# Kernel tuning notes

Measured on AMD Instinct MI355X. Metric: run time of the kernel, lower is better.

## Reference

```python
import jax, jax.numpy as jnp
import numpy as np

D_MODEL = 1024
N_HEADS = 16
HEAD_DIM = D_MODEL // N_HEADS  # 64
GRID = 8  # 8x8 Ising grid over head_dim pixels
N_DIFF_STEPS = 2
STEPS_PER_SAMPLE = 8  # cfg sampling.steps_per_sample
BETA_START = 0.8
BETA_END = 1.2


def setup_inputs() -> dict:
    key = jax.random.key(0)
    k1, k2, k3 = jax.random.split(key, 3)
    B, N = 4, 4096
    q = jax.random.normal(k1, (B, N, D_MODEL), dtype=jnp.float32)
    k = jax.random.normal(k2, (B, N, D_MODEL), dtype=jnp.float32)
    v = jax.random.normal(k3, (B, N, D_MODEL), dtype=jnp.float32)
    return {"q": q, "k": k, "v": v}


def _nbr_field(s):
    # s: (..., G, G) spins in {-1, +1}; 4-neighbor sum with open (non-torus) boundary
    zr = jnp.zeros_like(s[..., :1, :])
    zc = jnp.zeros_like(s[..., :, :1])
    up = jnp.concatenate([s[..., 1:, :], zr], axis=-2)
    down = jnp.concatenate([zr, s[..., :-1, :]], axis=-2)
    left = jnp.concatenate([s[..., :, 1:], zc], axis=-1)
    right = jnp.concatenate([zc, s[..., :, :-1]], axis=-1)
    return up + down + left + right


def _fta_forward(v):
    B, N, D = v.shape
    H, HD = N_HEADS, HEAD_DIM
    # binarize values -> Ising spins per head: (B, H, N, G, G)
    vh = v.reshape(B, N, H, HD).transpose(0, 2, 1, 3)
    spins = jnp.where(vh > 0, 1.0, -1.0).astype(jnp.float32).reshape(B, H, N, GRID, GRID)

    # log-spaced beta schedule (diffusion_schedule kind='log'), each diffusion
    # step runs STEPS_PER_SAMPLE Gibbs sweeps
    betas = jnp.exp(jnp.linspace(jnp.log(BETA_START), jnp.log(BETA_END), N_DIFF_STEPS))
    betas = jnp.repeat(betas, STEPS_PER_SAMPLE)  # (T,)
    T = N_DIFF_STEPS * STEPS_PER_SAMPLE

    ii, jj = jnp.meshgrid(jnp.arange(GRID), jnp.arange(GRID), indexing="ij")
    parity = ((ii + jj) % 2).astype(jnp.float32)  # checkerboard mask (G, G)

    keys = jax.random.split(jax.random.key(1234), T)

    def gibbs_step(s, xs):
        beta, kk = xs
        k0, k1 = jax.random.split(kk)

        def half_sweep(s, mask, kh):
            h = _nbr_field(s)
            p = jax.nn.sigmoid(2.0 * beta * h)  # P(spin=+1 | neighbors)
            u = jax.random.uniform(kh, s.shape, dtype=s.dtype)
            new = jnp.where(u < p, 1.0, -1.0)
            return jnp.where(mask > 0.5, new, s)

        s = half_sweep(s, parity, k0)
        s = half_sweep(s, 1.0 - parity, k1)
        return s, None

    spins, _ = jax.lax.scan(gibbs_step, spins, (betas, keys))

    # back to (B, N, D); spins already in {-1, +1} == bool*2-1
    out = spins.reshape(B, H, N, HD).transpose(0, 2, 1, 3).reshape(B, N, D)
    return out


def reference(q, k, v):
    # q and k are accepted for interface fidelity but, as in the source
    # module's head_fta, only v participates in the computation.
    return _fta_forward(v)
```

## Files before the change

kernel.cpp:

```cpp
#include <hip/hip_runtime.h>
#include <stdint.h>
#include <string.h>
#include <math.h>


struct FtaParams {
  uint32_t hk[32][2];
  uint32_t K9[2][9];
};

static inline void tf2x32_host(uint32_t k0, uint32_t k1, uint32_t c0, uint32_t c1,
                               uint32_t& o0, uint32_t& o1) {
  uint32_t ks2 = k0 ^ k1 ^ 0x1BD11BDAu;
  uint32_t x0 = c0 + k0, x1 = c1 + k1;
#define TFR(r) { x0 += x1; x1 = (x1 << (r)) | (x1 >> (32 - (r))); x1 ^= x0; }
  TFR(13) TFR(15) TFR(26) TFR(6)
  x0 += k1;  x1 += ks2 + 1u;
  TFR(17) TFR(29) TFR(16) TFR(24)
  x0 += ks2; x1 += k0 + 2u;
  TFR(13) TFR(15) TFR(26) TFR(6)
  x0 += k0;  x1 += k1 + 3u;
  TFR(17) TFR(29) TFR(16) TFR(24)
  x0 += k1;  x1 += ks2 + 4u;
  TFR(13) TFR(15) TFR(26) TFR(6)
  x0 += ks2; x1 += k0 + 5u;
#undef TFR
  o0 = x0; o1 = x1;
}

__device__ __forceinline__ static void tf_bits4(
    uint32_t K0, uint32_t K1, uint32_t ks2,
    uint32_t i1, uint32_t i2, uint32_t i3, uint32_t i4, uint32_t i5,
    uint32_t m0, uint32_t m1, uint32_t m2, uint32_t m3,
    uint32_t& o0, uint32_t& o1, uint32_t& o2, uint32_t& o3) {
#define ROTL(x, r) __builtin_amdgcn_alignbit((x), (x), 32u - (r))
#define QR4(r)                                                             \
  a0 += a1; b0 += b1; c0 += c1; d0 += d1;                                  \
  a1 = ROTL(a1, r) ^ a0; b1 = ROTL(b1, r) ^ b0;                            \
  c1 = ROTL(c1, r) ^ c0; d1 = ROTL(d1, r) ^ d0;
#define INJ4(sx, si)                                                       \
  a0 += sx; b0 += sx; c0 += sx; d0 += sx;                                  \
  a1 += si; b1 += si; c1 += si; d1 += si;
  uint32_t a1 = m0, b1 = m1, c1 = m2, d1 = m3;
  uint32_t a0 = K0 + a1, b0 = K0 + b1, c0 = K0 + c1, d0 = K0 + d1;
  a1 = ROTL(a1, 13) ^ a0; b1 = ROTL(b1, 13) ^ b0;
  c1 = ROTL(c1, 13) ^ c0; d1 = ROTL(d1, 13) ^ d0;
  QR4(15) QR4(26) QR4(6)
  INJ4(K1, i1)
  QR4(17) QR4(29) QR4(16) QR4(24)
  INJ4(ks2, i2)
  QR4(13) QR4(15) QR4(26) QR4(6)
  INJ4(K0, i3)
  QR4(17) QR4(29) QR4(16) QR4(24)
  INJ4(K1, i4)
  QR4(13) QR4(15) QR4(26) QR4(6)
  a0 += ks2; b0 += ks2; c0 += ks2; d0 += ks2;
  a1 += i5;  b1 += i5;  c1 += i5;  d1 += i5;
  o0 = a0 ^ a1; o1 = b0 ^ b1; o2 = c0 ^ c1; o3 = d0 ^ d1;
#undef QR4
#undef INJ4
#undef ROTL
}

__global__ __launch_bounds__(256, 8) void fta_kernel(const float* __restrict__ v,
                                                     float* __restrict__ out,
                                                     FtaParams P) {
  uint32_t tid = blockIdx.x * 256u + threadIdx.x;
  const int half = (int)(tid & 1u);
  uint32_t g = tid >> 1;
  uint32_t b = g >> 16;
  uint32_t h = (g >> 12) & 15u;
  uint32_t n = g & 4095u;

  size_t voff = ((size_t)(b * 4096u + n)) * 1024u + (size_t)h * 64u
              + (size_t)(half * 32);

  uint32_t nat = 0u;
#pragma unroll
  for (int k = 0; k < 32; k += 4) {
    float4 a = *reinterpret_cast<const float4*>(v + voff + k);
    nat |= ((uint32_t)(a.x > 0.0f)) << (k + 0);
    nat |= ((uint32_t)(a.y > 0.0f)) << (k + 1);
    nat |= ((uint32_t)(a.z > 0.0f)) << (k + 2);
    nat |= ((uint32_t)(a.w > 0.0f)) << (k + 3);
  }
  uint32_t bd = half ? __brev(nat) : nat;

  const uint32_t mgrid = g * 64u;
  const uint32_t mpc = mgrid + (half ? 63u : 0u);
  const int sgn = half ? -1 : 1;

  uint32_t K[9];
#pragma unroll
  for (int q = 0; q < 9; ++q) K[q] = P.K9[0][q];

  const uint32_t PM[2] = { 0x55AA55AAu, 0xAA55AA55u };

  for (int t = 0; t < 16; ++t) {
    if (t == 8) {
#pragma unroll
      for (int q = 0; q < 9; ++q) K[q] = P.K9[1][q];
    }
#pragma unroll
    for (int hf = 0; hf < 2; ++hf) {
      const uint32_t K0 = P.hk[2 * t + hf][0];
      const uint32_t K1 = P.hk[2 * t + hf][1];
      const uint32_t ks2 = K0 ^ K1 ^ 0x1BD11BDAu;
      const uint32_t i1 = ks2 + 1u, i2 = K0 + 2u, i3 = K1 + 3u,
                     i4 = ks2 + 4u, i5 = K0 + 5u;
      const uint32_t cKp = mpc + K1;

      uint32_t myrow3 = bd >> 24;
      uint32_t xrow = (uint32_t)__shfl_xor((int)myrow3, 1, 64);
      uint32_t xb = __brev(xrow) >> 24;

      uint32_t U  = (bd >> 8) | (xb << 24);
      uint32_t D  = bd << 8;
      uint32_t Lp = (bd >> 1) & 0x7f7f7f7fu;
      uint32_t Rp = (bd << 1) & 0xfefefefeu;
      uint32_t t0 = U ^ D,  ca = U & D;
      uint32_t t1 = Lp ^ Rp, cb = Lp & Rp;
      uint32_t c0 = t0 ^ t1, cc = t0 & t1;
      uint32_t cx = ca ^ cb;
      uint32_t c1 = cx ^ cc;
      uint32_t c2 = (ca & cb) | (cc & cx);

      uint32_t acc = 0u;
#pragma unroll
      for (int lr = 0; lr < 4; ++lr) {
        const int j0 = (lr + 1 + hf) & 1;
        const int L0 = lr * 8 + j0;
        uint32_t bits[4];
        tf_bits4(K0, K1, ks2, i1, i2, i3, i4, i5,
                 (uint32_t)((int)cKp + sgn * (L0 + 0)),
                 (uint32_t)((int)cKp + sgn * (L0 + 2)),
                 (uint32_t)((int)cKp + sgn * (L0 + 4)),
                 (uint32_t)((int)cKp + sgn * (L0 + 6)),
                 bits[0], bits[1], bits[2], bits[3]);
#pragma unroll
        for (int jj = 0; jj < 4; ++jj) {
          const int lc = j0 + 2 * jj;
          const int L = lr * 8 + lc;
          uint32_t b0v = (c0 >> L) & 1u;
          uint32_t b1v = (c1 >> L) & 1u;
          const int e = (int)(lr == 0) + (int)(lc == 0) + (int)(lc == 7);
          uint32_t thr;
          if (e == 0) {
            uint32_t b2v = (c2 >> L) & 1u;
            uint32_t tA = b0v ? K[2] : K[0];
            uint32_t tB = b0v ? K[6] : K[4];
            uint32_t tC = b1v ? tB : tA;
            thr = b2v ? K[8] : tC;
          } else if (e == 1) {
            uint32_t tA = b0v ? K[3] : K[1];
            uint32_t tB = b0v ? K[7] : K[5];
            thr = b1v ? tB : tA;
          } else {
            uint32_t tA = b0v ? K[4] : K[2];
            thr = b1v ? K[6] : tA;
          }
          uint32_t nb = (bits[jj] < thr) ? 1u : 0u;
          acc |= nb << L;
        }
      }
      bd = (bd & ~PM[hf]) | acc;
    }
  }

  uint32_t nato = half ? __brev(bd) : bd;
#pragma unroll
  for (int k = 0; k < 32; k += 4) {
    float4 o;
    o.x = ((nato >> (k + 0)) & 1u) ? 1.0f : -1.0f;
    o.y = ((nato >> (k + 1)) & 1u) ? 1.0f : -1.0f;
    o.z = ((nato >> (k + 2)) & 1u) ? 1.0f : -1.0f;
    o.w = ((nato >> (k + 3)) & 1u) ? 1.0f : -1.0f;
    *reinterpret_cast<float4*>(out + voff + k) = o;
  }
}

static float xla_expf(float xin) {
  const float exp_hi = 88.3762626647950f;
  const float exp_lo = -88.3762626647949f;
  const float LOG2EF = 1.44269504088896341f;
  const float C1 = 0.693359375f;
  const float C2 = -2.12194440e-4f;
  const float Pc0 = 1.9875691500E-4f;
  const float Pc1 = 1.3981999507E-3f;
  const float Pc2 = 8.3334519073E-3f;
  const float Pc3 = 4.1665795894E-2f;
  const float Pc4 = 1.6666665459E-1f;
  const float Pc5 = 5.0000001201E-1f;
#define MA(a, b, c) ((a) * (b) + (c))
  float x = xin;
  if (x > exp_hi) x = exp_hi;
  if (x < exp_lo) x = exp_lo;
  float fx = floorf(MA(x, LOG2EF, 0.5f));
  float tmp = C1 * fx;
  float z = C2 * fx;
  x = x - tmp;
  x = x - z;
  z = x * x;
  float y = MA(x, Pc0, Pc1);
  y = MA(y, x, Pc2);
  y = MA(y, x, Pc3);
  y = MA(y, x, Pc4);
  y = MA(y, x, Pc5);
  y = MA(y, z, x);
  y = y + 1.0f;
  int nn = (int)fx;
  uint32_t eb = (uint32_t)(nn + 127) << 23;
  float p2n;
  memcpy(&p2n, &eb, 4);
  float r = y * p2n;
  return r > xin ? r : xin;
#undef MA
}

extern "C" void kernel_launch(void* const* d_in, const int* in_sizes, int n_in,
                              void* d_out, int out_size, void* d_ws, size_t ws_size,
                              hipStream_t stream) {
  (void)in_sizes; (void)n_in; (void)d_ws; (void)ws_size; (void)out_size;
  const float* v = (const float*)d_in[2];
  float* out = (float*)d_out;

  FtaParams P;

  const uint32_t rk0 = 0u, rk1 = 1234u;
  uint32_t kt[16][2];
  for (uint32_t t = 0; t < 16; ++t) tf2x32_host(rk0, rk1, 0u, t, kt[t][0], kt[t][1]);
  for (int t = 0; t < 16; ++t) {
    uint32_t a0, a1, b0, b1;
    tf2x32_host(kt[t][0], kt[t][1], 0u, 0u, a0, a1);
    tf2x32_host(kt[t][0], kt[t][1], 0u, 1u, b0, b1);
    P.hk[2 * t + 0][0] = a0; P.hk[2 * t + 0][1] = a1;
    P.hk[2 * t + 1][0] = b0; P.hk[2 * t + 1][1] = b1;
  }

  float bet[2];
  bet[0] = (float)exp((double)(float)log((double)0.8f));
  bet[1] = (float)exp((double)(float)log((double)1.2f));

  for (int s = 0; s < 2; ++s) {
    float x2b = 2.0f * bet[s];
    for (int hh = -4; hh <= 4; ++hh) {
      float xh = x2b * (float)hh;
      float e = xla_expf(-xh);
      float p = 1.0f / (1.0f + e);
      double pd = (double)p * 8388608.0;
      uint64_t kc = (uint64_t)ceil(pd);
      uint64_t k9 = kc << 9;
      P.K9[s][hh + 4] = (k9 > 0xFFFFFFFFull) ? 0xFFFFFFFFu : (uint32_t)k9;
    }
  }

  fta_kernel<<<dim3(2048), dim3(256), 0, stream>>>(v, out, P);
}
```

Measured before the change: 529.8 us.

## Replace register-select threshold lookup with shared-memory table and roll inner loops

The nine per-beta thresholds move from registers and a select tree into a shared-memory table indexed by the neighbour-count bits plus an edge offset. The t, hf and lr loops are no longer unrolled, which shrinks the code and the register footprint. This is meant to cut the VALU select work and register pressure, at the cost of LDS loads on the threshold path, a syncthreads, and loop and address overhead that unrolling had removed.

```diff
diff --git a/kernel.cpp b/kernel.cpp
--- a/kernel.cpp
+++ b/kernel.cpp
@@ -65,6 +65,13 @@
 __global__ __launch_bounds__(256, 8) void fta_kernel(const float* __restrict__ v,
                                                      float* __restrict__ out,
                                                      FtaParams P) {
+  __shared__ uint32_t sK[18];
+  if (threadIdx.x == 0) {
+#pragma unroll
+    for (int q = 0; q < 18; ++q) sK[q] = P.K9[q / 9][q % 9];
+  }
+  __syncthreads();
+
   uint32_t tid = blockIdx.x * 256u + threadIdx.x;
   const int half = (int)(tid & 1u);
   uint32_t g = tid >> 1;
@@ -86,22 +93,13 @@
   }
   uint32_t bd = half ? __brev(nat) : nat;
 
-  const uint32_t mgrid = g * 64u;
-  const uint32_t mpc = mgrid + (half ? 63u : 0u);
+  const uint32_t mpc = g * 64u + (half ? 63u : 0u);
   const int sgn = half ? -1 : 1;
 
-  uint32_t K[9];
-#pragma unroll
-  for (int q = 0; q < 9; ++q) K[q] = P.K9[0][q];
-
-  const uint32_t PM[2] = { 0x55AA55AAu, 0xAA55AA55u };
-
+#pragma unroll 1
   for (int t = 0; t < 16; ++t) {
-    if (t == 8) {
-#pragma unroll
-      for (int q = 0; q < 9; ++q) K[q] = P.K9[1][q];
-    }
-#pragma unroll
+    const uint32_t koff = (t < 8) ? 0u : 9u;
+#pragma unroll 1
     for (int hf = 0; hf < 2; ++hf) {
       const uint32_t K0 = P.hk[2 * t + hf][0];
       const uint32_t K1 = P.hk[2 * t + hf][1];
@@ -109,6 +107,7 @@
       const uint32_t i1 = ks2 + 1u, i2 = K0 + 2u, i3 = K1 + 3u,
                      i4 = ks2 + 4u, i5 = K0 + 5u;
       const uint32_t cKp = mpc + K1;
+      const uint32_t pm = hf ? 0xAA55AA55u : 0x55AA55AAu;
 
       uint32_t myrow3 = bd >> 24;
       uint32_t xrow = (uint32_t)__shfl_xor((int)myrow3, 1, 64);
@@ -126,44 +125,45 @@
       uint32_t c2 = (ca & cb) | (cc & cx);
 
       uint32_t acc = 0u;
-#pragma unroll
+#pragma unroll 1
       for (int lr = 0; lr < 4; ++lr) {
-        const int j0 = (lr + 1 + hf) & 1;
-        const int L0 = lr * 8 + j0;
+        const uint32_t j0 = (uint32_t)((lr + 1 + hf) & 1);
+        const uint32_t L0 = (uint32_t)lr * 8u + j0;
+        const uint32_t e0 = (lr == 0) ? 1u : 0u;
+
+        uint32_t sb0 = 4u * (koff + e0 + (j0 == 0u ? 1u : 0u));
+        uint32_t sb1 = 4u * (koff + e0);
+        uint32_t sb2 = 4u * (koff + e0);
+        uint32_t sb3 = 4u * (koff + e0 + (j0 == 1u ? 1u : 0u));
+
+        const char* sKb = (const char*)sK;
+        uint32_t thr[4];
+#pragma unroll
+        for (int jj = 0; jj < 4; ++jj) {
+          uint32_t Lv = L0 + 2u * (uint32_t)jj;
+          uint32_t x = (c0 >> Lv) & 1u;
+          uint32_t y = (c1 >> Lv) & 1u;
+          uint32_t z = (c2 >> Lv) & 1u;
+          uint32_t sb = (jj == 0) ? sb0 : (jj == 1) ? sb1 : (jj == 2) ? sb2 : sb3;
+          uint32_t baddr = sb + 8u * x + 16u * y + 32u * z;
+          thr[jj] = *(const uint32_t*)(sKb + baddr);
+        }
+
         uint32_t bits[4];
         tf_bits4(K0, K1, ks2, i1, i2, i3, i4, i5,
-                 (uint32_t)((int)cKp + sgn * (L0 + 0)),
-                 (uint32_t)((int)cKp + sgn * (L0 + 2)),
-                 (uint32_t)((int)cKp + sgn * (L0 + 4)),
-                 (uint32_t)((int)cKp + sgn * (L0 + 6)),
+                 (uint32_t)((int)cKp + sgn * (int)(L0 + 0u)),
+                 (uint32_t)((int)cKp + sgn * (int)(L0 + 2u)),
+                 (uint32_t)((int)cKp + sgn * (int)(L0 + 4u)),
+                 (uint32_t)((int)cKp + sgn * (int)(L0 + 6u)),
                  bits[0], bits[1], bits[2], bits[3]);
+
 #pragma unroll
         for (int jj = 0; jj < 4; ++jj) {
-          const int lc = j0 + 2 * jj;
-          const int L = lr * 8 + lc;
-          uint32_t b0v = (c0 >> L) & 1u;
-          uint32_t b1v = (c1 >> L) & 1u;
-          const int e = (int)(lr == 0) + (int)(lc == 0) + (int)(lc == 7);
-          uint32_t thr;
-          if (e == 0) {
-            uint32_t b2v = (c2 >> L) & 1u;
-            uint32_t tA = b0v ? K[2] : K[0];
-            uint32_t tB = b0v ? K[6] : K[4];
-            uint32_t tC = b1v ? tB : tA;
-            thr = b2v ? K[8] : tC;
-          } else if (e == 1) {
-            uint32_t tA = b0v ? K[3] : K[1];
-            uint32_t tB = b0v ? K[7] : K[5];
-            thr = b1v ? tB : tA;
-          } else {
-            uint32_t tA = b0v ? K[4] : K[2];
-            thr = b1v ? K[6] : tA;
-          }
-          uint32_t nb = (bits[jj] < thr) ? 1u : 0u;
-          acc |= nb << L;
+          uint32_t Lv = L0 + 2u * (uint32_t)jj;
+          acc |= ((bits[jj] < thr[jj]) ? 1u : 0u) << Lv;
         }
       }
-      bd = (bd & ~PM[hf]) | acc;
+      bd = (bd & ~pm) | acc;
     }
   }
 
```

New measurement: 581.7 us. 9.8% more time.
